# Kernel optimization log

Measured on AMD Instinct MI355X. Metric: run time of the kernel, lower is better.

Reference implementation:

```python
import jax, jax.numpy as jnp
import numpy as np

PN, KN, MBON, DAN = 3, 50, 10, 10
DT = 0.5
TAU = 1.0          # kenyon/apl/mbon/dan tau
RC = 5.0           # kenyon & dan lowpass RC
TAU_W = 2.0        # mbon tau_weights


def setup_inputs() -> dict:
    key = jax.random.key(0)
    ks = jax.random.split(key, 16)
    T, B = 128, 32768
    n = lambda k, shape, s=0.5: jax.random.normal(k, shape, dtype=jnp.float32) * s
    return {
        "odor": jax.random.normal(ks[0], (T, B, PN), dtype=jnp.float32),
        "context": jax.random.uniform(ks[1], (T, B, 1), dtype=jnp.float32),
        # KenyonCell
        "pn_weight": n(ks[2], (B, PN, KN)),
        "kn_bias": n(ks[3], (KN,)),
        # APLCell
        "apl_kc_weight": jnp.ones((KN, 1), dtype=jnp.float32),
        "apl_bias": jnp.full((1,), -0.5, dtype=jnp.float32),
        # MBONCell
        "mbon_dan_weight": n(ks[4], (DAN, MBON)),
        "mbon_bias": n(ks[5], (MBON,)),
        # DANCell
        "dan_mbon_weight": n(ks[6], (MBON, DAN)),
        "dan_dan_weight": n(ks[7], (DAN, DAN)),
        "dan_context_weight": n(ks[8], (1, DAN)),
        "dan_bias": n(ks[9], (DAN,)),
        # decoder Linear(10, 2)
        "dec_W": n(ks[10], (2, MBON), 0.3),
        "dec_b": n(ks[11], (2,), 0.1),
        # plastic KC->MBON weights and their activation trace
        "kc_weight0": n(ks[12], (B, KN, MBON)),
        "wact0": jnp.zeros((B, KN, MBON), dtype=jnp.float32),
    }


def _run(odor, context, pn_weight, kn_bias, apl_kc_weight, apl_bias,
         mbon_dan_weight, mbon_bias, dan_mbon_weight, dan_dan_weight,
         dan_context_weight, dan_bias, dec_W, dec_b, kc_weight0, wact0):
    B = odor.shape[1]
    dt_tau = DT / TAU
    alpha = DT / (DT + RC)          # lowpass coefficient (same RC for KC and DAN)
    dt_tauw = DT / TAU_W
    relu = jax.nn.relu

    def step(carry, xs):
        kc, apl, mbon, dan, low_kc, low_dan, kc_w, wact = carry
        odor_t, ctx_t = xs            # [B,PN], [B,1]
        # KenyonCell: per-batch PN->KC matmul, APL inhibition (ones weight -> broadcast)
        pn_value = jnp.einsum('bp,bpk->bk', odor_t, pn_weight)      # [B,KN]
        kc_n = kc * (1 - dt_tau) + dt_tau * relu(pn_value - apl + kn_bias)
        # APLCell
        apl_n = apl * (1 - dt_tau) + dt_tau * relu(kc_n @ apl_kc_weight + apl_bias)
        # MBONCell: plastic per-batch KC->MBON weights, DAN gating
        kc_value = jnp.einsum('bk,bkm->bm', kc_n, kc_w)             # [B,MBON]
        dan_mod = jax.nn.sigmoid(dan @ mbon_dan_weight)             # [B,MBON]
        mbon_n = mbon * (1 - dt_tau) + dt_tau * dan_mod * relu(kc_value + mbon_bias)
        # DANCell
        dan_pre = dan @ dan_dan_weight + mbon_n @ dan_mbon_weight + ctx_t @ dan_context_weight + dan_bias
        dan_n = dan * (1 - dt_tau) + dt_tau * relu(dan_pre)
        # low-pass traces
        low_kc_n = alpha * kc_n + (1 - alpha) * low_kc
        low_dan_n = alpha * dan_n + (1 - alpha) * low_dan
        # plasticity: weights blend toward OLD activation trace, trace integrates new activity
        syn = kc_n[:, :, None] * low_dan_n[:, None, :] - low_kc[:, :, None] * dan_n[:, None, :]
        # note: torch code uses state_low_kc AFTER update -> low_kc_n; keep faithful:
        syn = kc_n[:, :, None] * low_dan_n[:, None, :] - low_kc_n[:, :, None] * dan_n[:, None, :]
        wact_n = wact + DT * syn
        kc_w_n = kc_w * (1 - dt_tauw) + dt_tauw * wact
        out = mbon_n @ dec_W.T + dec_b                              # [B,2]
        return (kc_n, apl_n, mbon_n, dan_n, low_kc_n, low_dan_n, kc_w_n, wact_n), out

    z = lambda *s: jnp.zeros(s, dtype=jnp.float32)
    carry0 = (z(B, KN), z(B, 1), z(B, MBON), z(B, DAN), z(B, KN), z(B, DAN), kc_weight0, wact0)
    _, outs = jax.lax.scan(step, carry0, (odor, context))
    return outs                                                     # [T,B,2]


def reference(odor, context, pn_weight, kn_bias, apl_kc_weight, apl_bias,
              mbon_dan_weight, mbon_bias, dan_mbon_weight, dan_dan_weight,
              dan_context_weight, dan_bias, dec_W, dec_b, kc_weight0, wact0):
    return _run(odor, context, pn_weight, kn_bias, apl_kc_weight, apl_bias,
                mbon_dan_weight, mbon_bias, dan_mbon_weight, dan_dan_weight,
                dan_context_weight, dan_bias, dec_W, dec_b, kc_weight0, wact0)
```

## Files before the change

### kernel.cpp

```cpp
#include <hip/hip_runtime.h>

#define KN  50
#define NM  10
#define LPB 16

typedef float v2f __attribute__((ext_vector_type(2)));

template <int CTRL>
__device__ __forceinline__ float dpp_add(float x) {
  return x + __int_as_float(
      __builtin_amdgcn_update_dpp(0, __float_as_int(x), CTRL, 0xF, 0xF, true));
}

__device__ __forceinline__ float rowsum16(float x) {
  x = dpp_add<0x121>(x);
  x = dpp_add<0x122>(x);
  x = dpp_add<0x124>(x);
  x = dpp_add<0x128>(x);
  return x;
}

extern "C" __global__ void __launch_bounds__(256)
__attribute__((amdgpu_waves_per_eu(2, 2)))
fly_kernel(const float* __restrict__ odor,
           const float* __restrict__ ctxp,
           const float* __restrict__ pn_w,
           const float* __restrict__ kn_b,
           const float* __restrict__ apl_w,
           const float* __restrict__ apl_b,
           const float* __restrict__ mdw_g,
           const float* __restrict__ mbon_b,
           const float* __restrict__ dmw_g,
           const float* __restrict__ ddw_g,
           const float* __restrict__ dcw_g,
           const float* __restrict__ dan_b,
           const float* __restrict__ decW,
           const float* __restrict__ decb,
           const float* __restrict__ kcw0,
           const float* __restrict__ wact0,
           float* __restrict__ out,
           int B, int T)
{
  __shared__ float smb[16][16];
  __shared__ float sdn[16][16];

  const int tid   = threadIdx.x;
  const int j     = tid & (LPB - 1);
  const int jhalf = j >> 1;
  const int jodd  = j & 1;
  const int g     = tid >> 4;
  const int b     = blockIdx.x * (256 / LPB) + g;
  if (b >= B) return;

  const bool has4 = (j + 48) < KN;

  v2f   kcw[4][5], wct[4][5];
  float pw0[4], pw1[4], pw2[4], knb[4], aw[4];
  float kcn[4] = {0.f,0.f,0.f,0.f}, lkc[4] = {0.f,0.f,0.f,0.f};

  #pragma unroll
  for (int i = 0; i < 4; ++i) {
    const int k = j + 16 * i;
    if (i < 3 || has4) {
      const v2f* a = reinterpret_cast<const v2f*>(kcw0  + ((size_t)b * KN + k) * NM);
      const v2f* w = reinterpret_cast<const v2f*>(wact0 + ((size_t)b * KN + k) * NM);
      #pragma unroll
      for (int h = 0; h < 5; ++h) { kcw[i][h] = a[h]; wct[i][h] = 0.25f * w[h]; }
      pw0[i] = pn_w[((size_t)b * 3 + 0) * KN + k];
      pw1[i] = pn_w[((size_t)b * 3 + 1) * KN + k];
      pw2[i] = pn_w[((size_t)b * 3 + 2) * KN + k];
      knb[i] = kn_b[k];
      aw[i]  = apl_w[k];
    } else {
      #pragma unroll
      for (int h = 0; h < 5; ++h) { kcw[i][h] = (v2f)(0.f); wct[i][h] = (v2f)(0.f); }
      pw0[i] = pw1[i] = pw2[i] = 0.f; knb[i] = 0.f; aw[i] = 0.f;
    }
  }

  v2f   mdw2[5], ddw2[5], dmw2[5];
  float cw = 0.f, db_ = 0.f, mb_ = 0.f, dw0 = 0.f, dw1 = 0.f;
  #pragma unroll
  for (int h = 0; h < 5; ++h) { mdw2[h] = (v2f)(0.f); ddw2[h] = (v2f)(0.f); dmw2[h] = (v2f)(0.f); }
  if (j < NM) {
    #pragma unroll
    for (int h = 0; h < 5; ++h) {
      mdw2[h].x = mdw_g[(2*h)   * NM + j];  mdw2[h].y = mdw_g[(2*h+1) * NM + j];
      ddw2[h].x = ddw_g[(2*h)   * NM + j];  ddw2[h].y = ddw_g[(2*h+1) * NM + j];
      dmw2[h].x = dmw_g[(2*h)   * NM + j];  dmw2[h].y = dmw_g[(2*h+1) * NM + j];
    }
    cw  = dcw_g[j];
    db_ = dan_b[j];
    mb_ = mbon_b[j];
    dw0 = decW[j];
    dw1 = decW[NM + j];
  }
  const float aplb = apl_b[0];
  const float db0 = decb[0], db1 = decb[1];

  const float ALPHA = (float)(0.5 / 5.5);

  float apl = 0.f, mbon_m = 0.f, dan_m = 0.f;
  v2f dvec2[5], ldv2[5];
  #pragma unroll
  for (int h = 0; h < 5; ++h) { dvec2[h] = (v2f)(0.f); ldv2[h] = (v2f)(0.f); }

  const float* op = odor + (size_t)b * 3;
  const float* cp = ctxp + b;
  const size_t so = (size_t)B * 3;
  float o0n = op[0], o1n = op[1], o2n = op[2];
  float cxn = *cp;

  for (int t = 0; t < T; ++t) {
    const float o0 = o0n, o1 = o1n, o2 = o2n, cx = cxn;
    if (t + 1 < T) {
      op += so; cp += B;
      o0n = op[0]; o1n = op[1]; o2n = op[2]; cxn = *cp;
    }

    float psum = 0.f;
    v2f p2[5];
    #pragma unroll
    for (int h = 0; h < 5; ++h) p2[h] = (v2f)(0.f);

    #pragma unroll
    for (int i = 0; i < 4; ++i) {
      if (i < 3 || has4) {
        const float base = knb[i] - apl;
        float pv = fmaf(pw0[i], o0, fmaf(pw1[i], o1, fmaf(pw2[i], o2, base)));
        float r  = fmaxf(pv, 0.f);
        float kn = 0.5f * (kcn[i] + r);
        kcn[i] = kn;
        lkc[i] = fmaf(ALPHA, kn - lkc[i], lkc[i]);
        psum = fmaf(kn, aw[i], psum);
        #pragma unroll
        for (int h = 0; h < 5; ++h) p2[h] += kn * kcw[i][h];
      }
    }

    psum = rowsum16(psum);
    #pragma unroll
    for (int h = 0; h < 5; ++h) {
      p2[h].x = rowsum16(p2[h].x);
      p2[h].y = rowsum16(p2[h].y);
    }

    apl = 0.5f * apl + 0.5f * fmaxf(psum + aplb, 0.f);

    v2f rsel = p2[0];
    #pragma unroll
    for (int h = 1; h < 5; ++h) rsel = (jhalf == h) ? p2[h] : rsel;
    const float kcv = jodd ? rsel.y : rsel.x;

    v2f s2 = dvec2[0] * mdw2[0];
    #pragma unroll
    for (int e = 1; e < 5; ++e) s2 += dvec2[e] * mdw2[e];
    const float s = s2.x + s2.y;
    const float dmod = 1.f / (1.f + __expf(-s));
    mbon_m = 0.5f * mbon_m + 0.5f * dmod * fmaxf(kcv + mb_, 0.f);
    smb[g][j] = mbon_m;

    v2f acc = dvec2[0] * ddw2[0];
    #pragma unroll
    for (int e = 1; e < 5; ++e) acc += dvec2[e] * ddw2[e];
    {
      const v2f* pm = reinterpret_cast<const v2f*>(&smb[g][0]);
      #pragma unroll
      for (int h = 0; h < 5; ++h) acc += pm[h] * dmw2[h];
    }
    float dp = acc.x + acc.y + fmaf(cx, cw, db_);
    dan_m = 0.5f * dan_m + 0.5f * fmaxf(dp, 0.f);
    sdn[g][j] = dan_m;

    {
      const v2f* pd = reinterpret_cast<const v2f*>(&sdn[g][0]);
      #pragma unroll
      for (int e = 0; e < 5; ++e) {
        dvec2[e] = pd[e];
        ldv2[e] += ALPHA * (dvec2[e] - ldv2[e]);
      }
    }

    const float q0 = rowsum16(mbon_m * dw0) + db0;
    const float q1 = rowsum16(mbon_m * dw1) + db1;
    if (j == 0) {
      float2 st; st.x = q0; st.y = q1;
      *reinterpret_cast<float2*>(out + ((size_t)t * B + b) * 2) = st;
    }

    #pragma unroll
    for (int i = 0; i < 4; ++i) {
      if (i < 3 || has4) {
        const float kh  =  0.125f * kcn[i];
        const float nlh = -0.125f * lkc[i];
        #pragma unroll
        for (int h = 0; h < 5; ++h) {
          const v2f w = wct[i][h];
          kcw[i][h] = 0.75f * kcw[i][h] + w;
          wct[i][h] = w + kh * ldv2[h] + nlh * dvec2[h];
        }
      }
    }
  }
}

extern "C" void kernel_launch(void* const* d_in, const int* in_sizes, int n_in,
                              void* d_out, int out_size, void* d_ws, size_t ws_size,
                              hipStream_t stream) {
  const float* odor   = (const float*)d_in[0];
  const float* ctx    = (const float*)d_in[1];
  const float* pn_w   = (const float*)d_in[2];
  const float* kn_b   = (const float*)d_in[3];
  const float* apl_w  = (const float*)d_in[4];
  const float* apl_b  = (const float*)d_in[5];
  const float* mdw    = (const float*)d_in[6];
  const float* mbon_b = (const float*)d_in[7];
  const float* dmw    = (const float*)d_in[8];
  const float* ddw    = (const float*)d_in[9];
  const float* dcw    = (const float*)d_in[10];
  const float* dan_b  = (const float*)d_in[11];
  const float* decW   = (const float*)d_in[12];
  const float* decb   = (const float*)d_in[13];
  const float* kcw0   = (const float*)d_in[14];
  const float* wact0  = (const float*)d_in[15];
  float* out = (float*)d_out;

  const int B = in_sizes[14] / (KN * NM);
  const int T = in_sizes[0] / (B * 3);

  const int batches_per_block = 256 / LPB;
  dim3 grid((B + batches_per_block - 1) / batches_per_block);
  dim3 block(256);
  hipLaunchKernelGGL(fly_kernel, grid, block, 0, stream,
                     odor, ctx, pn_w, kn_b, apl_w, apl_b,
                     mdw, mbon_b, dmw, ddw, dcw, dan_b,
                     decW, decb, kcw0, wact0, out, B, T);
}
```

Measured before the change: 892.6 us.

## Replace LDS exchange of MBON/DAN state with DPP row reductions

Drops the shared-memory arrays used to broadcast MBON and DAN activations within each 16-lane group. Each lane now contributes its own row-weighted terms, with lane 10 carrying the context weight and DAN bias, and DPP rowsum16 reductions give every lane the full DAN pre-activation vector. Every lane then updates its dvec/low-pass copy redundantly in registers. This removes the LDS store/load round trips on the serial time-step dependency chain, at the cost of ten extra row reductions and some extra VALU work per step.

```diff
diff --git a/kernel.cpp b/kernel.cpp
--- a/kernel.cpp
+++ b/kernel.cpp
@@ -41,18 +41,15 @@
            float* __restrict__ out,
            int B, int T)
 {
-  __shared__ float smb[16][16];
-  __shared__ float sdn[16][16];
-
   const int tid   = threadIdx.x;
   const int j     = tid & (LPB - 1);
   const int jhalf = j >> 1;
   const int jodd  = j & 1;
-  const int g     = tid >> 4;
-  const int b     = blockIdx.x * (256 / LPB) + g;
+  const int b     = blockIdx.x * (256 / LPB) + (tid >> 4);
   if (b >= B) return;
 
-  const bool has4 = (j + 48) < KN;
+  const bool has4  = (j + 48) < KN;
+  const bool isl10 = (j == 10);
 
   v2f   kcw[4][5], wct[4][5];
   float pw0[4], pw1[4], pw2[4], knb[4], aw[4];
@@ -78,22 +75,26 @@
     }
   }
 
-  v2f   mdw2[5], ddw2[5], dmw2[5];
-  float cw = 0.f, db_ = 0.f, mb_ = 0.f, dw0 = 0.f, dw1 = 0.f;
+  v2f   mdw2[5], ddwr[5], dmwr[5];
+  float mb_ = 0.f, dw0 = 0.f, dw1 = 0.f;
   #pragma unroll
-  for (int h = 0; h < 5; ++h) { mdw2[h] = (v2f)(0.f); ddw2[h] = (v2f)(0.f); dmw2[h] = (v2f)(0.f); }
+  for (int h = 0; h < 5; ++h) { mdw2[h] = (v2f)(0.f); ddwr[h] = (v2f)(0.f); dmwr[h] = (v2f)(0.f); }
   if (j < NM) {
     #pragma unroll
     for (int h = 0; h < 5; ++h) {
       mdw2[h].x = mdw_g[(2*h)   * NM + j];  mdw2[h].y = mdw_g[(2*h+1) * NM + j];
-      ddw2[h].x = ddw_g[(2*h)   * NM + j];  ddw2[h].y = ddw_g[(2*h+1) * NM + j];
-      dmw2[h].x = dmw_g[(2*h)   * NM + j];  dmw2[h].y = dmw_g[(2*h+1) * NM + j];
-    }
-    cw  = dcw_g[j];
-    db_ = dan_b[j];
+      ddwr[h].x = ddw_g[j * NM + 2*h];      ddwr[h].y = ddw_g[j * NM + 2*h + 1];
+      dmwr[h].x = dmw_g[j * NM + 2*h];      dmwr[h].y = dmw_g[j * NM + 2*h + 1];
+    }
     mb_ = mbon_b[j];
     dw0 = decW[j];
     dw1 = decW[NM + j];
+  } else if (isl10) {
+    #pragma unroll
+    for (int h = 0; h < 5; ++h) {
+      ddwr[h].x = dcw_g[2*h];   ddwr[h].y = dcw_g[2*h + 1];
+      dmwr[h].x = dan_b[2*h];   dmwr[h].y = dan_b[2*h + 1];
+    }
   }
   const float aplb = apl_b[0];
   const float db0 = decb[0], db1 = decb[1];
@@ -158,27 +159,31 @@
     const float s = s2.x + s2.y;
     const float dmod = 1.f / (1.f + __expf(-s));
     mbon_m = 0.5f * mbon_m + 0.5f * dmod * fmaxf(kcv + mb_, 0.f);
-    smb[g][j] = mbon_m;
-
-    v2f acc = dvec2[0] * ddw2[0];
-    #pragma unroll
-    for (int e = 1; e < 5; ++e) acc += dvec2[e] * ddw2[e];
-    {
-      const v2f* pm = reinterpret_cast<const v2f*>(&smb[g][0]);
-      #pragma unroll
-      for (int h = 0; h < 5; ++h) acc += pm[h] * dmw2[h];
-    }
-    float dp = acc.x + acc.y + fmaf(cx, cw, db_);
-    dan_m = 0.5f * dan_m + 0.5f * fmaxf(dp, 0.f);
-    sdn[g][j] = dan_m;
-
-    {
-      const v2f* pd = reinterpret_cast<const v2f*>(&sdn[g][0]);
-      #pragma unroll
-      for (int e = 0; e < 5; ++e) {
-        dvec2[e] = pd[e];
-        ldv2[e] += ALPHA * (dvec2[e] - ldv2[e]);
-      }
+
+    const float du = isl10 ? cx  : dan_m;
+    const float mu = isl10 ? 1.f : mbon_m;
+    v2f c2[5];
+    #pragma unroll
+    for (int h = 0; h < 5; ++h) c2[h] = du * ddwr[h] + mu * dmwr[h];
+    #pragma unroll
+    for (int h = 0; h < 5; ++h) {
+      c2[h].x = rowsum16(c2[h].x);
+      c2[h].y = rowsum16(c2[h].y);
+    }
+
+    v2f rs2 = c2[0];
+    #pragma unroll
+    for (int h = 1; h < 5; ++h) rs2 = (jhalf == h) ? c2[h] : rs2;
+    const float dpj = jodd ? rs2.y : rs2.x;
+    dan_m = 0.5f * dan_m + 0.5f * fmaxf(dpj, 0.f);
+
+    #pragma unroll
+    for (int h = 0; h < 5; ++h) {
+      v2f dn;
+      dn.x = fmaxf(c2[h].x, 0.f);
+      dn.y = fmaxf(c2[h].y, 0.f);
+      dvec2[h] = 0.5f * dvec2[h] + 0.5f * dn;
+      ldv2[h] += ALPHA * (dvec2[h] - ldv2[h]);
     }
 
     const float q0 = rowsum16(mbon_m * dw0) + db0;
```

After: 968.7 us. 8.5% more time.
